# Optimization experiments

Measured on AMD Instinct MI355X. Metric: run time of the kernel, lower is better.

Reference implementation:

```python
import jax, jax.numpy as jnp
import numpy as np

E = 128       # estimators
R = 65536     # regions per estimator
S = 100000    # update samples


def setup_inputs() -> dict:
    key = jax.random.key(0)
    k1, k2, k3, k4, k5 = jax.random.split(key, 5)
    a = jax.random.uniform(k1, (E, R), dtype=jnp.float32) + 0.1
    b = jax.random.uniform(k2, (E, R), dtype=jnp.float32) + 0.1
    samples_regions = jax.random.randint(k3, (S, E), 0, R, dtype=jnp.int32)
    da = jax.random.uniform(k4, (S,), dtype=jnp.float32)
    db = jax.random.uniform(k5, (S,), dtype=jnp.float32)
    return {"a": a, "b": b, "samples_regions": samples_regions, "da": da, "db": db}


def reference(a, b, samples_regions, da, db):
    # Original: lax.scan over samples, each step vmapping over estimators and
    # doing beliefs.a.at[region].add(da). Addition is commutative, so the whole
    # scan is a single batched scatter-add into the [E, R] tables.
    est = jnp.arange(a.shape[0], dtype=samples_regions.dtype)[None, :]  # [1, E]
    new_a = a.at[est, samples_regions].add(da[:, None])  # indices broadcast to [S, E]
    new_b = b.at[est, samples_regions].add(db[:, None])
    return jnp.stack([new_a, new_b])  # [2, E, R]
```

## Files before the change

### kernel.cpp

```cpp
#include <hip/hip_runtime.h>

#define NE 128
#define NR 65536
#define NS 100000
#define NSP 100096
#define CHUNK 16384
#define NCHUNK (NR / CHUNK)

#define FXSCALE 67108864.0f
#define FXINV   1.4901161193847656e-8f

typedef float vfloat4 __attribute__((ext_vector_type(4)));

__global__ __launch_bounds__(256) void EnsembleBeliefs_transpose(
    const int* __restrict__ in,
    int* __restrict__ outT)
{
    __shared__ int tile[64 * 133];
    const int t  = threadIdx.x;
    const int s0 = blockIdx.x * 64;

#pragma unroll
    for (int k = 0; k < 8; ++k) {
        const int idx = k * 256 + t;
        const int sl  = idx >> 5;
        const int c4  = idx & 31;
        const int s   = s0 + sl;
        if (s < NS) {
            const int4 v = *(const int4*)(in + (size_t)s * NE + 4 * c4);
            const int o = sl * 133 + 4 * c4;
            tile[o] = v.x; tile[o + 1] = v.y; tile[o + 2] = v.z; tile[o + 3] = v.w;
        }
    }
    __syncthreads();

#pragma unroll
    for (int k = 0; k < 8; ++k) {
        const int idx = k * 256 + t;
        const int e = idx >> 4;
        const int c = idx & 15;
        int4 v;
        v.x = tile[(4 * c + 0) * 133 + e];
        v.y = tile[(4 * c + 1) * 133 + e];
        v.z = tile[(4 * c + 2) * 133 + e];
        v.w = tile[(4 * c + 3) * 133 + e];
        *(int4*)(outT + (size_t)e * NSP + s0 + 4 * c) = v;
    }
}

#define FXQ(vv) ((unsigned)__builtin_fmaf((vv), FXSCALE, 0.5f))
#define HIST_AT(rr, qq)                                                        \
    { int _rl = (rr) - base; if ((unsigned)_rl < (unsigned)CHUNK) atomicAdd(&h[_rl], (qq)); }

__global__ __launch_bounds__(1024, 8) void EnsembleBeliefs_hist(
    const int* __restrict__ regT,
    const float* __restrict__ da,
    const float* __restrict__ db,
    const float* __restrict__ a,
    const float* __restrict__ b,
    float* __restrict__ out)
{
    __shared__ unsigned h[CHUNK];
    const int e    = blockIdx.x;
    const int tb   = blockIdx.y >> 2;
    const int base = (blockIdx.y & 3) << 14;
    const int tid  = threadIdx.x;

    uint4* h4 = (uint4*)h;
    for (int j = tid; j < CHUNK / 4; j += 1024) h4[j] = make_uint4(0u, 0u, 0u, 0u);
    __syncthreads();

    const int4*   reg4 = (const int4*)(regT + (size_t)e * NSP);
    const float4* v4   = (const float4*)(tb ? db : da);
    const int n4 = NS / 4;

    for (int i = tid; i + 3 * 1024 < n4; i += 4 * 1024) {
        const int4   r0 = reg4[i];
        const int4   r1 = reg4[i + 1024];
        const int4   r2 = reg4[i + 2048];
        const int4   r3 = reg4[i + 3072];
        const float4 v0 = v4[i];
        const float4 v1 = v4[i + 1024];
        const float4 v2 = v4[i + 2048];
        const float4 v3 = v4[i + 3072];
        HIST_AT(r0.x, FXQ(v0.x)) HIST_AT(r0.y, FXQ(v0.y)) HIST_AT(r0.z, FXQ(v0.z)) HIST_AT(r0.w, FXQ(v0.w))
        HIST_AT(r1.x, FXQ(v1.x)) HIST_AT(r1.y, FXQ(v1.y)) HIST_AT(r1.z, FXQ(v1.z)) HIST_AT(r1.w, FXQ(v1.w))
        HIST_AT(r2.x, FXQ(v2.x)) HIST_AT(r2.y, FXQ(v2.y)) HIST_AT(r2.z, FXQ(v2.z)) HIST_AT(r2.w, FXQ(v2.w))
        HIST_AT(r3.x, FXQ(v3.x)) HIST_AT(r3.y, FXQ(v3.y)) HIST_AT(r3.z, FXQ(v3.z)) HIST_AT(r3.w, FXQ(v3.w))
    }
    for (int i = 24576 + tid; i < n4; i += 1024) {
        const int4   r = reg4[i];
        const float4 v = v4[i];
        HIST_AT(r.x, FXQ(v.x)) HIST_AT(r.y, FXQ(v.y)) HIST_AT(r.z, FXQ(v.z)) HIST_AT(r.w, FXQ(v.w))
    }
    __syncthreads();

    const size_t off = ((size_t)e << 16) + (size_t)base;
    const vfloat4* src4 = (const vfloat4*)((tb ? b : a) + off);
    vfloat4*       dst4 = (vfloat4*)(out + ((size_t)tb << 23) + off);
    for (int j = tid; j < CHUNK / 4; j += 1024) {
        const vfloat4 s = __builtin_nontemporal_load(src4 + j);
        const uint4 x = h4[j];
        vfloat4 o;
        o.x = __builtin_fmaf((float)x.x, FXINV, s.x);
        o.y = __builtin_fmaf((float)x.y, FXINV, s.y);
        o.z = __builtin_fmaf((float)x.z, FXINV, s.z);
        o.w = __builtin_fmaf((float)x.w, FXINV, s.w);
        __builtin_nontemporal_store(o, dst4 + j);
    }
}

__global__ __launch_bounds__(256) void EnsembleBeliefs_scatter(
    const int* __restrict__ regions,
    const float* __restrict__ da,
    const float* __restrict__ db,
    float* __restrict__ out)
{
    const int idx = blockIdx.x * 256 + threadIdx.x;
    const int s = idx >> 7;
    const int e = idx & (NE - 1);
    const int region = regions[idx];
    const size_t off = ((size_t)e << 16) + (size_t)region;
    atomicAdd(out + off, da[s]);
    atomicAdd(out + ((size_t)NE << 16) + off, db[s]);
}

extern "C" void kernel_launch(void* const* d_in, const int* in_sizes, int n_in,
                              void* d_out, int out_size, void* d_ws, size_t ws_size,
                              hipStream_t stream) {
    const float* a       = (const float*)d_in[0];
    const float* b       = (const float*)d_in[1];
    const int*   regions = (const int*)  d_in[2];
    const float* da      = (const float*)d_in[3];
    const float* db      = (const float*)d_in[4];
    float* out = (float*)d_out;

    const size_t regT_bytes = (size_t)NE * NSP * sizeof(int);

    if (ws_size >= regT_bytes) {
        int* regT = (int*)d_ws;
        EnsembleBeliefs_transpose<<<(NS + 63) / 64, 256, 0, stream>>>(regions, regT);
        dim3 hgrid(NE, 2 * NCHUNK);
        EnsembleBeliefs_hist<<<hgrid, 1024, 0, stream>>>(regT, da, db, a, b, out);
    } else {
        const size_t tbl_elems = (size_t)NE * NR;
        (void)hipMemcpyAsync(out, a, tbl_elems * sizeof(float), hipMemcpyDeviceToDevice, stream);
        (void)hipMemcpyAsync(out + tbl_elems, b, tbl_elems * sizeof(float), hipMemcpyDeviceToDevice, stream);
        EnsembleBeliefs_scatter<<<(NS * NE) / 256, 256, 0, stream>>>(regions, da, db, out);
    }
}
```

Before: 203.0 us.

## Pack a and b histogram counts into 64-bit LDS atomics in one pass

Adds a histogram kernel that accumulates both the da and db fixed-point increments into a single 64-bit shared-memory counter per region. Each block then handles both tables for its chunk, which halves the number of blocks that re-read the transposed region indices and halves the LDS atomic count. In exchange it uses 128KB of dynamic LDS per block, needing an attribute opt-in and lowering occupancy, and it relies on each 32-bit half not carrying into the other.

Result: no change. 200.4 us (-1.3%).

```diff
diff --git a/kernel.cpp b/kernel.cpp
--- a/kernel.cpp
+++ b/kernel.cpp
@@ -4,8 +4,11 @@
 #define NR 65536
 #define NS 100000
 #define NSP 100096
+
 #define CHUNK 16384
 #define NCHUNK (NR / CHUNK)
+
+#define CHUNK3 16384
 
 #define FXSCALE 67108864.0f
 #define FXINV   1.4901161193847656e-8f
@@ -49,6 +52,87 @@
 }
 
 #define FXQ(vv) ((unsigned)__builtin_fmaf((vv), FXSCALE, 0.5f))
+
+#define HIST3_AT(rr, fa, fb)                                                   \
+    { int _rl = (rr) - base;                                                   \
+      if ((unsigned)_rl < (unsigned)CHUNK3)                                    \
+          atomicAdd(&h64[_rl], (unsigned long long)FXQ(fa) |                   \
+                               ((unsigned long long)FXQ(fb) << 32)); }
+
+__global__ __launch_bounds__(1024, 4) void EnsembleBeliefs_hist3(
+    const int* __restrict__ regT,
+    const float* __restrict__ da,
+    const float* __restrict__ db,
+    const float* __restrict__ a,
+    const float* __restrict__ b,
+    float* __restrict__ out)
+{
+    extern __shared__ unsigned long long h64[];
+    const int e    = blockIdx.x;
+    const int base = blockIdx.y << 14;
+    const int tid  = threadIdx.x;
+
+    uint4* h4 = (uint4*)h64;
+    for (int j = tid; j < CHUNK3 * 2 / 4; j += 1024) h4[j] = make_uint4(0u, 0u, 0u, 0u);
+    __syncthreads();
+
+    const int4*   reg4 = (const int4*)(regT + (size_t)e * NSP);
+    const float4* a4   = (const float4*)da;
+    const float4* b4   = (const float4*)db;
+    const int n4 = NS / 4;
+
+    for (int i = tid; i + 3 * 1024 < n4; i += 4 * 1024) {
+        int4   r[4];
+        float4 va[4], vb[4];
+#pragma unroll
+        for (int k = 0; k < 4; ++k) r[k] = reg4[i + k * 1024];
+#pragma unroll
+        for (int k = 0; k < 4; ++k) va[k] = a4[i + k * 1024];
+#pragma unroll
+        for (int k = 0; k < 4; ++k) vb[k] = b4[i + k * 1024];
+        __builtin_amdgcn_sched_barrier(0);
+#pragma unroll
+        for (int k = 0; k < 4; ++k) {
+            HIST3_AT(r[k].x, va[k].x, vb[k].x)
+            HIST3_AT(r[k].y, va[k].y, vb[k].y)
+            HIST3_AT(r[k].z, va[k].z, vb[k].z)
+            HIST3_AT(r[k].w, va[k].w, vb[k].w)
+        }
+    }
+    for (int i = 24576 + tid; i < n4; i += 1024) {
+        const int4   r  = reg4[i];
+        const float4 va = a4[i];
+        const float4 vb = b4[i];
+        HIST3_AT(r.x, va.x, vb.x) HIST3_AT(r.y, va.y, vb.y)
+        HIST3_AT(r.z, va.z, vb.z) HIST3_AT(r.w, va.w, vb.w)
+    }
+    __syncthreads();
+
+    const size_t off = ((size_t)e << 16) + (size_t)base;
+    const vfloat4* srcA = (const vfloat4*)(a + off);
+    const vfloat4* srcB = (const vfloat4*)(b + off);
+    vfloat4* dstA = (vfloat4*)(out + off);
+    vfloat4* dstB = (vfloat4*)(out + (((size_t)NE << 16)) + off);
+    const uint4* hh = (const uint4*)h64;
+    for (int j = tid; j < CHUNK3 / 4; j += 1024) {
+        const uint4 p0 = hh[2 * j];
+        const uint4 p1 = hh[2 * j + 1];
+        const vfloat4 sa = __builtin_nontemporal_load(srcA + j);
+        const vfloat4 sb = __builtin_nontemporal_load(srcB + j);
+        vfloat4 oa, ob;
+        oa.x = __builtin_fmaf((float)p0.x, FXINV, sa.x);
+        ob.x = __builtin_fmaf((float)p0.y, FXINV, sb.x);
+        oa.y = __builtin_fmaf((float)p0.z, FXINV, sa.y);
+        ob.y = __builtin_fmaf((float)p0.w, FXINV, sb.y);
+        oa.z = __builtin_fmaf((float)p1.x, FXINV, sa.z);
+        ob.z = __builtin_fmaf((float)p1.y, FXINV, sb.z);
+        oa.w = __builtin_fmaf((float)p1.z, FXINV, sa.w);
+        ob.w = __builtin_fmaf((float)p1.w, FXINV, sb.w);
+        __builtin_nontemporal_store(oa, dstA + j);
+        __builtin_nontemporal_store(ob, dstB + j);
+    }
+}
+
 #define HIST_AT(rr, qq)                                                        \
     { int _rl = (rr) - base; if ((unsigned)_rl < (unsigned)CHUNK) atomicAdd(&h[_rl], (qq)); }
 
@@ -140,8 +224,23 @@
     if (ws_size >= regT_bytes) {
         int* regT = (int*)d_ws;
         EnsembleBeliefs_transpose<<<(NS + 63) / 64, 256, 0, stream>>>(regions, regT);
-        dim3 hgrid(NE, 2 * NCHUNK);
-        EnsembleBeliefs_hist<<<hgrid, 1024, 0, stream>>>(regT, da, db, a, b, out);
+
+        static int big_lds = -1;
+        if (big_lds < 0) {
+            big_lds = (hipFuncSetAttribute(
+                           reinterpret_cast<const void*>(EnsembleBeliefs_hist3),
+                           hipFuncAttributeMaxDynamicSharedMemorySize,
+                           CHUNK3 * (int)sizeof(unsigned long long)) == hipSuccess) ? 1 : 0;
+        }
+
+        if (big_lds) {
+            dim3 hgrid(NE, 4);
+            EnsembleBeliefs_hist3<<<hgrid, 1024, CHUNK3 * sizeof(unsigned long long), stream>>>(
+                regT, da, db, a, b, out);
+        } else {
+            dim3 hgrid(NE, 2 * NCHUNK);
+            EnsembleBeliefs_hist<<<hgrid, 1024, 0, stream>>>(regT, da, db, a, b, out);
+        }
     } else {
         const size_t tbl_elems = (size_t)NE * NR;
         (void)hipMemcpyAsync(out, a, tbl_elems * sizeof(float), hipMemcpyDeviceToDevice, stream);
```
